# Performance work log

Measured on AMD Instinct MI355X. Metric: run time of the kernel, lower is better.

Reference implementation:

```python
import jax, jax.numpy as jnp
import numpy as np

D_STATE = 16


def setup_inputs() -> dict:
    key = jax.random.key(0)
    ks = jax.random.split(key, 7)
    B, S, D = 8, 4096, 64
    ds = D_STATE
    x = jax.random.normal(ks[0], (B, S, D), dtype=jnp.float32)
    # Selection layers modeled as Linear(d_model, out). W_A scaled small so the
    # random transition matrices are contractive over 4096 steps.
    W_A = jax.random.normal(ks[1], (D, ds * ds), dtype=jnp.float32) * 0.01
    b_A = jnp.zeros((ds * ds,), dtype=jnp.float32)
    W_B = jax.random.normal(ks[2], (D, ds * D), dtype=jnp.float32) * 0.05
    b_B = jnp.zeros((ds * D,), dtype=jnp.float32)
    W_C = jax.random.normal(ks[3], (D, ds * D), dtype=jnp.float32) * 0.05
    b_C = jnp.zeros((ds * D,), dtype=jnp.float32)
    return {"x": x, "W_A": W_A, "b_A": b_A, "W_B": W_B, "b_B": b_B,
            "W_C": W_C, "b_C": b_C}


def reference(x, W_A, b_A, W_B, b_B, W_C, b_C):
    B, S, D = x.shape
    ds = D_STATE
    # Input-dependent (selective) parameters per timestep
    A = (x @ W_A + b_A).reshape(B, S, ds, ds)      # [B,S,ds,ds]
    Bm = (x @ W_B + b_B).reshape(B, S, ds, D)      # [B,S,ds,D]
    Cm = (x @ W_C + b_C).reshape(B, S, ds, D)      # [B,S,ds,D]
    # Pre-contract B_t @ x_t once: [B,S,ds]
    Bx = jnp.einsum('bsnd,bsd->bsn', Bm, x)

    def step(h, inputs):
        A_t, Bx_t = inputs                          # [B,ds,ds], [B,ds]
        h = jnp.einsum('bij,bj->bi', A_t, h) + Bx_t
        return h, h

    h0 = jnp.zeros((B, ds), dtype=x.dtype)
    _, hs = jax.lax.scan(step, h0,
                         (jnp.swapaxes(A, 0, 1), jnp.swapaxes(Bx, 0, 1)))
    hs = jnp.swapaxes(hs, 0, 1)                     # [B,S,ds]
    # output_t = C_t^T @ h_t  -> [B,S,D]
    return jnp.einsum('bsnd,bsn->bsd', Cm, hs)
```

## Files before the change

### kernel.cpp

```cpp
#include <hip/hip_runtime.h>

#define BATCH   8
#define SEQ     4096
#define DM      64
#define DS      16
#define BS      (BATCH*SEQ)
#define CHUNK   16
#define NCHT    (BS/CHUNK)
#define SG      16
#define NSG     (NCHT/SG)

typedef __attribute__((ext_vector_type(8))) __bf16 bf16x8;
typedef __attribute__((ext_vector_type(4))) float  f32x4;

__device__ __forceinline__ unsigned short f2bf(float f) {
  unsigned int u = __float_as_uint(f);
  u += 0x7fffu + ((u >> 16) & 1u);
  return (unsigned short)(u >> 16);
}
__device__ __forceinline__ float bflo(unsigned int u) { return __uint_as_float(u << 16); }
__device__ __forceinline__ float bfhi(unsigned int u) { return __uint_as_float(u & 0xffff0000u); }

#define AS_I 20
#define AS_T 324

__global__ __launch_bounds__(256) void k0_castw(
    const float* __restrict__ WA, const float* __restrict__ WB,
    const float* __restrict__ WC,
    unsigned short* __restrict__ WAt, unsigned short* __restrict__ WBt,
    unsigned short* __restrict__ WCt)
{
  const int o = blockIdx.x * 256 + threadIdx.x;
  if (o < 16384) {
    const int c = o >> 6, e = o & 63;
    WAt[o] = f2bf(WA[e * 256 + c]);
  } else if (o < 16384 + 65536) {
    const int p = o - 16384;
    const int c = p >> 6, e = p & 63;
    WBt[p] = f2bf(WB[e * 1024 + c]);
  } else {
    const int p = o - 16384 - 65536;
    const int c = p >> 6, e = p & 63;
    WCt[p] = f2bf(WC[e * 1024 + c]);
  }
}

__global__ __launch_bounds__(128) void g1(
    const float* __restrict__ x, const unsigned short* __restrict__ WBt,
    const float* __restrict__ bB, const unsigned short* __restrict__ WAt,
    const float* __restrict__ bA, unsigned short* __restrict__ xb,
    unsigned short* __restrict__ Wt_ws, float* __restrict__ u_ws,
    float* __restrict__ P_ws, float* __restrict__ v_ws)
{
  __shared__ __align__(16) unsigned char smem[32 * AS_T * 2];
  float (*xs)[68]     = (float (*)[68])smem;
  float* bBs          = (float*)(smem + 8704);
  unsigned short* As  = (unsigned short*)smem;
  __shared__ __align__(16) float bxs[32][16];
  __shared__ __align__(16) float us[2][16];

  const int tid  = threadIdx.x;
  const int lane = tid & 63;
  const int l15  = lane & 15;
  const int quad = lane >> 4;
  const int w    = tid >> 6;
  const int t0   = blockIdx.x * 32;
  const int twl  = w * 16;

  {
    const float4* xg = (const float4*)(x + (size_t)t0 * DM);
    #pragma unroll
    for (int i = 0; i < 4; ++i) {
      const int f4 = tid + 128 * i;
      ((float4*)&xs[f4 >> 4][0])[f4 & 15] = xg[f4];
    }
    ((float4*)bBs)[tid]       = ((const float4*)bB)[tid];
    ((float4*)bBs)[tid + 128] = ((const float4*)bB)[tid + 128];
    if (tid < 32) us[tid >> 4][tid & 15] = 0.f;
  }
  __syncthreads();

  bf16x8 a0, a1;
  {
    const int row = twl + l15;
    union { bf16x8 v; ushort4 s[2]; } ua, ub;
    float4 p0 = *(const float4*)&xs[row][quad * 8];
    float4 p1 = *(const float4*)&xs[row][quad * 8 + 4];
    float4 p2 = *(const float4*)&xs[row][32 + quad * 8];
    float4 p3 = *(const float4*)&xs[row][32 + quad * 8 + 4];
    ua.s[0] = (ushort4){f2bf(p0.x), f2bf(p0.y), f2bf(p0.z), f2bf(p0.w)};
    ua.s[1] = (ushort4){f2bf(p1.x), f2bf(p1.y), f2bf(p1.z), f2bf(p1.w)};
    ub.s[0] = (ushort4){f2bf(p2.x), f2bf(p2.y), f2bf(p2.z), f2bf(p2.w)};
    ub.s[1] = (ushort4){f2bf(p3.x), f2bf(p3.y), f2bf(p3.z), f2bf(p3.w)};
    a0 = ua.v; a1 = ub.v;
    unsigned short* xp = xb + (size_t)(t0 + row) * 64 + quad * 8;
    *(bf16x8*)xp        = a0;
    *(bf16x8*)(xp + 32) = a1;
  }

  #pragma unroll 2
  for (int n = 0; n < 16; ++n) {
    f32x4 ac[4];
    #pragma unroll
    for (int r = 0; r < 4; ++r) {
      const bf16x8* wv = (const bf16x8*)(WBt + (size_t)((n * 4 + r) * 16 + l15) * 64);
      f32x4 t = {0.f, 0.f, 0.f, 0.f};
      t = __builtin_amdgcn_mfma_f32_16x16x32_bf16(a0, wv[quad],     t, 0, 0, 0);
      t = __builtin_amdgcn_mfma_f32_16x16x32_bf16(a1, wv[quad + 4], t, 0, 0, 0);
      ac[r] = t;
    }
    float part[4] = {0.f, 0.f, 0.f, 0.f};
    #pragma unroll
    for (int r = 0; r < 4; ++r) {
      const float bb = bBs[n * 64 + r * 16 + l15];
      #pragma unroll
      for (int reg = 0; reg < 4; ++reg) {
        const int tl = twl + quad * 4 + reg;
        part[reg] = fmaf(ac[r][reg] + bb, xs[tl][r * 16 + l15], part[reg]);
      }
    }
    #pragma unroll
    for (int off = 1; off < 16; off <<= 1) {
      #pragma unroll
      for (int reg = 0; reg < 4; ++reg)
        part[reg] += __shfl_xor(part[reg], off, 64);
    }
    if (l15 == 0) {
      #pragma unroll
      for (int reg = 0; reg < 4; ++reg)
        bxs[twl + quad * 4 + reg][n] = part[reg];
    }
  }
  __syncthreads();

  #pragma unroll 2
  for (int ns = 0; ns < 16; ++ns) {
    const bf16x8* wv = (const bf16x8*)(WAt + (size_t)(ns * 16 + l15) * 64);
    f32x4 acc = {0.f, 0.f, 0.f, 0.f};
    acc = __builtin_amdgcn_mfma_f32_16x16x32_bf16(a0, wv[quad],     acc, 0, 0, 0);
    acc = __builtin_amdgcn_mfma_f32_16x16x32_bf16(a1, wv[quad + 4], acc, 0, 0, 0);
    const float bias = bA[ns * 16 + l15];
    #pragma unroll
    for (int r = 0; r < 4; ++r)
      As[(twl + quad * 4 + r) * AS_T + ns * AS_I + l15] = f2bf(acc[r] + bias);
  }
  __syncthreads();

  {
    bf16x8 wb;
    #pragma unroll
    for (int j = 0; j < 8; ++j) wb[j] = (__bf16)((quad * 8 + j == l15) ? 1.f : 0.f);
    f32x4 d = {0.f, 0.f, 0.f, 0.f};
    const int qq = quad & 1;

    #pragma unroll 1
    for (int t = 0; t < CHUNK; ++t) {
      const int tl = twl + t;
      const unsigned short* rp = &As[tl * AS_T + l15 * AS_I];
      uint2 r0 = *(const uint2*)(rp);
      uint2 r1 = *(const uint2*)(rp + 4);
      uint2 r2 = *(const uint2*)(rp + 8);
      uint2 r3 = *(const uint2*)(rp + 12);

      uint4 abits;
      if (quad == 0)      abits = make_uint4(r0.x, r0.y, r1.x, r1.y);
      else if (quad == 1) abits = make_uint4(r2.x, r2.y, r3.x, r3.y);
      else                abits = make_uint4(0u, 0u, 0u, 0u);
      bf16x8 af = *(bf16x8*)&abits;

      f32x4 z4 = {0.f, 0.f, 0.f, 0.f};
      d = __builtin_amdgcn_mfma_f32_16x16x32_bf16(af, wb, z4, 0, 0, 0);

      float nu = bxs[tl][l15];
      {
        float4 U0 = *(const float4*)&us[w][0];
        float4 U1 = *(const float4*)&us[w][4];
        float4 U2 = *(const float4*)&us[w][8];
        float4 U3 = *(const float4*)&us[w][12];
        nu = fmaf(bflo(r0.x), U0.x, nu); nu = fmaf(bfhi(r0.x), U0.y, nu);
        nu = fmaf(bflo(r0.y), U0.z, nu); nu = fmaf(bfhi(r0.y), U0.w, nu);
        nu = fmaf(bflo(r1.x), U1.x, nu); nu = fmaf(bfhi(r1.x), U1.y, nu);
        nu = fmaf(bflo(r1.y), U1.z, nu); nu = fmaf(bfhi(r1.y), U1.w, nu);
        nu = fmaf(bflo(r2.x), U2.x, nu); nu = fmaf(bfhi(r2.x), U2.y, nu);
        nu = fmaf(bflo(r2.y), U2.z, nu); nu = fmaf(bfhi(r2.y), U2.w, nu);
        nu = fmaf(bflo(r3.x), U3.x, nu); nu = fmaf(bfhi(r3.x), U3.y, nu);
        nu = fmaf(bflo(r3.y), U3.z, nu); nu = fmaf(bfhi(r3.y), U3.w, nu);
      }

      bf16x8 nb;
      nb[0] = (__bf16)__shfl(d[0], (2 * qq + 0) * 16 + l15, 64);
      nb[1] = (__bf16)__shfl(d[1], (2 * qq + 0) * 16 + l15, 64);
      nb[2] = (__bf16)__shfl(d[2], (2 * qq + 0) * 16 + l15, 64);
      nb[3] = (__bf16)__shfl(d[3], (2 * qq + 0) * 16 + l15, 64);
      nb[4] = (__bf16)__shfl(d[0], (2 * qq + 1) * 16 + l15, 64);
      nb[5] = (__bf16)__shfl(d[1], (2 * qq + 1) * 16 + l15, 64);
      nb[6] = (__bf16)__shfl(d[2], (2 * qq + 1) * 16 + l15, 64);
      nb[7] = (__bf16)__shfl(d[3], (2 * qq + 1) * 16 + l15, 64);
      wb = nb;

      if (quad == 0) {
        us[w][l15] = nu;
        bxs[tl][l15] = nu;
      }
      #pragma unroll
      for (int r = 0; r < 4; ++r)
        As[tl * AS_T + (quad * 4 + r) * AS_I + l15] = f2bf(d[r]);
    }

    const int chunk = blockIdx.x * 2 + w;
    #pragma unroll
    for (int r = 0; r < 4; ++r)
      P_ws[(size_t)chunk * 256 + (quad * 4 + r) * 16 + l15] = d[r];
    if (quad == 0) v_ws[(size_t)chunk * DS + l15] = us[w][l15];
  }
  __syncthreads();

  {
    uint4* Wg = (uint4*)(Wt_ws + (size_t)t0 * 256);
    #pragma unroll 1
    for (int z = 0; z < 8; ++z) {
      const int p4 = z * 128 + tid;
      const int f  = p4 * 8;
      const int t  = f >> 8, i = (f >> 4) & 15, k = f & 15;
      const unsigned short* sp = &As[t * AS_T + i * AS_I + k];
      uint2 lo = *(const uint2*)(sp);
      uint2 hi = *(const uint2*)(sp + 4);
      Wg[p4] = make_uint4(lo.x, lo.y, hi.x, hi.y);
    }
    ((float4*)(u_ws + (size_t)t0 * DS))[tid] = ((const float4*)&bxs[0][0])[tid];
  }
}

__global__ __launch_bounds__(256) void k3a(
    const float* __restrict__ P_ws, const float* __restrict__ v_ws,
    float* __restrict__ Q_ws, float* __restrict__ w_ws)
{
  __shared__ float wsv[4][16];
  const int tid  = threadIdx.x;
  const int lane = tid & 63;
  const int l15  = lane & 15;
  const int quad = lane >> 4;
  const int wv   = tid >> 6;
  const int s    = blockIdx.x * 4 + wv;
  const int qq   = quad & 1;

  if (lane < 16) wsv[wv][lane] = 0.f;
  bf16x8 wb;
  #pragma unroll
  for (int j = 0; j < 8; ++j) wb[j] = (__bf16)((quad * 8 + j == l15) ? 1.f : 0.f);
  f32x4 d = {0.f, 0.f, 0.f, 0.f};

  #pragma unroll 1
  for (int t = 0; t < SG; ++t) {
    const int chunk = s * SG + t;
    float4 p0 = {0.f,0.f,0.f,0.f}, p1 = {0.f,0.f,0.f,0.f};
    if (quad < 2) {
      const float4* pr = (const float4*)(P_ws + (size_t)chunk * 256 + l15 * 16 + quad * 8);
      p0 = pr[0]; p1 = pr[1];
    }
    bf16x8 af;
    af[0] = (__bf16)p0.x; af[1] = (__bf16)p0.y; af[2] = (__bf16)p0.z; af[3] = (__bf16)p0.w;
    af[4] = (__bf16)p1.x; af[5] = (__bf16)p1.y; af[6] = (__bf16)p1.z; af[7] = (__bf16)p1.w;

    f32x4 z4 = {0.f, 0.f, 0.f, 0.f};
    d = __builtin_amdgcn_mfma_f32_16x16x32_bf16(af, wb, z4, 0, 0, 0);

    float part = 0.f;
    if (quad < 2) {
      const float* wrow = &wsv[wv][quad * 8];
      part = p0.x*wrow[0] + p0.y*wrow[1] + p0.z*wrow[2] + p0.w*wrow[3]
           + p1.x*wrow[4] + p1.y*wrow[5] + p1.z*wrow[6] + p1.w*wrow[7];
    }
    part += __shfl_xor(part, 16, 64);
    const float nv = v_ws[(size_t)chunk * DS + l15];

    bf16x8 nb;
    nb[0] = (__bf16)__shfl(d[0], (2 * qq + 0) * 16 + l15, 64);
    nb[1] = (__bf16)__shfl(d[1], (2 * qq + 0) * 16 + l15, 64);
    nb[2] = (__bf16)__shfl(d[2], (2 * qq + 0) * 16 + l15, 64);
    nb[3] = (__bf16)__shfl(d[3], (2 * qq + 0) * 16 + l15, 64);
    nb[4] = (__bf16)__shfl(d[0], (2 * qq + 1) * 16 + l15, 64);
    nb[5] = (__bf16)__shfl(d[1], (2 * qq + 1) * 16 + l15, 64);
    nb[6] = (__bf16)__shfl(d[2], (2 * qq + 1) * 16 + l15, 64);
    nb[7] = (__bf16)__shfl(d[3], (2 * qq + 1) * 16 + l15, 64);
    wb = nb;

    if (quad == 0) wsv[wv][l15] = part + nv;
  }

  #pragma unroll
  for (int r = 0; r < 4; ++r)
    Q_ws[(size_t)s * 256 + (quad * 4 + r) * 16 + l15] = d[r];
  if (quad == 0) w_ws[(size_t)s * DS + l15] = wsv[wv][l15];
}

__global__ __launch_bounds__(128) void k3b(
    const float* __restrict__ Q_ws, const float* __restrict__ w_ws,
    float* __restrict__ hbg_ws)
{
  const int tid = threadIdx.x;
  const int b = tid >> 4;
  const int r = tid & 15;
  float h = 0.f;

  #pragma unroll 1
  for (int g = 0; g < 16; ++g) {
    const int s = b * 16 + g;
    const float4* Pr = (const float4*)&Q_ws[(size_t)s * 256 + r * 16];
    float4 c0 = Pr[0], c1 = Pr[1], c2 = Pr[2], c3 = Pr[3];
    const float vc = w_ws[(size_t)s * DS + r];
    hbg_ws[(size_t)s * DS + r] = h;
    float acc = vc;
    acc += c0.x*__shfl(h, 0,16) + c0.y*__shfl(h, 1,16) + c0.z*__shfl(h, 2,16) + c0.w*__shfl(h, 3,16);
    acc += c1.x*__shfl(h, 4,16) + c1.y*__shfl(h, 5,16) + c1.z*__shfl(h, 6,16) + c1.w*__shfl(h, 7,16);
    acc += c2.x*__shfl(h, 8,16) + c2.y*__shfl(h, 9,16) + c2.z*__shfl(h,10,16) + c2.w*__shfl(h,11,16);
    acc += c3.x*__shfl(h,12,16) + c3.y*__shfl(h,13,16) + c3.z*__shfl(h,14,16) + c3.w*__shfl(h,15,16);
    h = acc;
  }
}

__global__ __launch_bounds__(256) void k3c(
    const float* __restrict__ P_ws, const float* __restrict__ v_ws,
    const float* __restrict__ hbg_ws, float* __restrict__ hb_ws)
{
  const int tid = threadIdx.x;
  const int s = blockIdx.x * 16 + (tid >> 4);
  const int r = tid & 15;
  float h = hbg_ws[(size_t)s * DS + r];

  #pragma unroll 1
  for (int t = 0; t < SG; ++t) {
    const int chunk = s * SG + t;
    const float4* Pr = (const float4*)&P_ws[(size_t)chunk * 256 + r * 16];
    float4 c0 = Pr[0], c1 = Pr[1], c2 = Pr[2], c3 = Pr[3];
    const float vc = v_ws[(size_t)chunk * DS + r];
    hb_ws[(size_t)chunk * DS + r] = h;
    float acc = vc;
    acc += c0.x*__shfl(h, 0,16) + c0.y*__shfl(h, 1,16) + c0.z*__shfl(h, 2,16) + c0.w*__shfl(h, 3,16);
    acc += c1.x*__shfl(h, 4,16) + c1.y*__shfl(h, 5,16) + c1.z*__shfl(h, 6,16) + c1.w*__shfl(h, 7,16);
    acc += c2.x*__shfl(h, 8,16) + c2.y*__shfl(h, 9,16) + c2.z*__shfl(h,10,16) + c2.w*__shfl(h,11,16);
    acc += c3.x*__shfl(h,12,16) + c3.y*__shfl(h,13,16) + c3.z*__shfl(h,14,16) + c3.w*__shfl(h,15,16);
    h = acc;
  }
}

__global__ __launch_bounds__(256) void g2(
    const unsigned short* __restrict__ xb, const unsigned short* __restrict__ WCt,
    const float* __restrict__ bC, const unsigned short* __restrict__ Wt_ws,
    const float* __restrict__ u_ws, const float* __restrict__ hb_ws,
    float* __restrict__ out)
{
  __shared__ float hsh[64][17];
  __shared__ float bCs[1024];
  const int tid  = threadIdx.x;
  const int lane = tid & 63;
  const int l15  = lane & 15;
  const int quad = lane >> 4;
  const int w    = tid >> 6;
  const int t0   = blockIdx.x * 64;
  const int twl  = w * 16;

  ((float4*)bCs)[tid] = ((const float4*)bC)[tid];

  #pragma unroll
  for (int z = 0; z < 4; ++z) {
    const int gcell = z * 256 + tid;
    const int tl = gcell >> 4, i = gcell & 15;
    const int t = t0 + tl;
    const uint4* wr = (const uint4*)(Wt_ws + (size_t)t * 256 + i * 16);
    uint4 wa = wr[0], wbv = wr[1];
    const float4* hp = (const float4*)(hb_ws + (size_t)(t >> 4) * DS);
    float4 h0 = hp[0], h1 = hp[1], h2 = hp[2], h3 = hp[3];
    float acc = u_ws[(size_t)t * DS + i];
    acc = fmaf(bflo(wa.x),  h0.x, acc); acc = fmaf(bfhi(wa.x),  h0.y, acc);
    acc = fmaf(bflo(wa.y),  h0.z, acc); acc = fmaf(bfhi(wa.y),  h0.w, acc);
    acc = fmaf(bflo(wa.z),  h1.x, acc); acc = fmaf(bfhi(wa.z),  h1.y, acc);
    acc = fmaf(bflo(wa.w),  h1.z, acc); acc = fmaf(bfhi(wa.w),  h1.w, acc);
    acc = fmaf(bflo(wbv.x), h2.x, acc); acc = fmaf(bfhi(wbv.x), h2.y, acc);
    acc = fmaf(bflo(wbv.y), h2.z, acc); acc = fmaf(bfhi(wbv.y), h2.w, acc);
    acc = fmaf(bflo(wbv.z), h3.x, acc); acc = fmaf(bfhi(wbv.z), h3.y, acc);
    acc = fmaf(bflo(wbv.w), h3.z, acc); acc = fmaf(bfhi(wbv.w), h3.w, acc);
    hsh[tl][i] = acc;
  }

  const bf16x8* xv = (const bf16x8*)(xb + (size_t)(t0 + twl + l15) * 64);
  bf16x8 a0 = xv[quad];
  bf16x8 a1 = xv[quad + 4];
  __syncthreads();

  f32x4 ota[4];
  #pragma unroll
  for (int r = 0; r < 4; ++r) ota[r] = (f32x4){0.f, 0.f, 0.f, 0.f};

  #pragma unroll 2
  for (int n = 0; n < 16; ++n) {
    f32x4 ac[4];
    #pragma unroll
    for (int r = 0; r < 4; ++r) {
      const bf16x8* wv = (const bf16x8*)(WCt + (size_t)((n * 4 + r) * 16 + l15) * 64);
      f32x4 t = {0.f, 0.f, 0.f, 0.f};
      t = __builtin_amdgcn_mfma_f32_16x16x32_bf16(a0, wv[quad],     t, 0, 0, 0);
      t = __builtin_amdgcn_mfma_f32_16x16x32_bf16(a1, wv[quad + 4], t, 0, 0, 0);
      ac[r] = t;
    }
    float hn[4];
    #pragma unroll
    for (int reg = 0; reg < 4; ++reg) hn[reg] = hsh[twl + quad * 4 + reg][n];
    #pragma unroll
    for (int r = 0; r < 4; ++r) {
      const float bc = bCs[n * 64 + r * 16 + l15];
      #pragma unroll
      for (int reg = 0; reg < 4; ++reg)
        ota[r][reg] = fmaf(ac[r][reg] + bc, hn[reg], ota[r][reg]);
    }
  }

  #pragma unroll
  for (int r = 0; r < 4; ++r)
    #pragma unroll
    for (int reg = 0; reg < 4; ++reg)
      out[(size_t)(t0 + twl + quad * 4 + reg) * DM + r * 16 + l15] = ota[r][reg];
}

extern "C" void kernel_launch(void* const* d_in, const int* in_sizes, int n_in,
                              void* d_out, int out_size, void* d_ws, size_t ws_size,
                              hipStream_t stream) {
  const float* x  = (const float*)d_in[0];
  const float* WA = (const float*)d_in[1];
  const float* bA = (const float*)d_in[2];
  const float* WB = (const float*)d_in[3];
  const float* bB = (const float*)d_in[4];
  const float* WC = (const float*)d_in[5];
  const float* bC = (const float*)d_in[6];
  float* out = (float*)d_out;

  float* ws     = (float*)d_ws;
  float* P_ws   = ws;
  float* v_ws   = P_ws   + (size_t)NCHT * 256;
  float* u_ws   = v_ws   + (size_t)NCHT * DS;
  float* Q_ws   = u_ws   + (size_t)BS * DS;
  float* w_ws   = Q_ws   + (size_t)NSG * 256;
  float* hbg_ws = w_ws   + (size_t)NSG * DS;
  float* hb_ws  = hbg_ws + (size_t)NSG * DS;
  unsigned short* xb    = (unsigned short*)(hb_ws + (size_t)NCHT * DS);
  unsigned short* WAt   = xb  + (size_t)BS * 64;
  unsigned short* WBt   = WAt + 256 * 64;
  unsigned short* WCt   = WBt + 1024 * 64;
  unsigned short* Wt_ws = WCt + 1024 * 64;

  k0_castw<<<576,      256, 0, stream>>>(WA, WB, WC, WAt, WBt, WCt);
  g1      <<<BS / 32,  128, 0, stream>>>(x, WBt, bB, WAt, bA, xb, Wt_ws, u_ws, P_ws, v_ws);
  k3a     <<<NSG / 4,  256, 0, stream>>>(P_ws, v_ws, Q_ws, w_ws);
  k3b     <<<1,        128, 0, stream>>>(Q_ws, w_ws, hbg_ws);
  k3c     <<<NSG / 16, 256, 0, stream>>>(P_ws, v_ws, hbg_ws, hb_ws);
  g2      <<<BS / 64,  256, 0, stream>>>(xb, WCt, bC, Wt_ws, u_ws, hb_ws, out);
}
```

Baseline: 182.7 us.

## Software-pipeline weight and state loads across all kernels, fuse A and B projection loops

Adds register double-buffering of weight fragments in g1 and g2, so the next iteration's global loads are issued before the current MFMAs, and merges the A-projection loop into the B loop in g1, which removes a barrier. The scan kernels (g1 inner loop, k3a, k3b, k3c) prefetch the next step's operands and split serial FMA chains into independent partial sums to shorten the dependency chain. Launch bounds change occupancy hints, and g1's shared memory is no longer aliased, which raises LDS use. The risks are higher register pressure and changed floating-point summation order.

```diff
diff --git a/kernel.cpp b/kernel.cpp
--- a/kernel.cpp
+++ b/kernel.cpp
@@ -45,17 +45,41 @@
   }
 }
 
-__global__ __launch_bounds__(128) void g1(
+struct WFrag {
+  bf16x8 b00, b01, b10, b11, b20, b21, b30, b31;
+  bf16x8 a0f, a1f;
+  float  ba;
+};
+
+__device__ __forceinline__ WFrag loadw(
+    const unsigned short* __restrict__ WBt, const unsigned short* __restrict__ WAt,
+    const float* __restrict__ bA, int n, int l15, int quad)
+{
+  WFrag f;
+  const bf16x8* w0 = (const bf16x8*)(WBt + (size_t)((n * 4 + 0) * 16 + l15) * 64);
+  const bf16x8* w1 = (const bf16x8*)(WBt + (size_t)((n * 4 + 1) * 16 + l15) * 64);
+  const bf16x8* w2 = (const bf16x8*)(WBt + (size_t)((n * 4 + 2) * 16 + l15) * 64);
+  const bf16x8* w3 = (const bf16x8*)(WBt + (size_t)((n * 4 + 3) * 16 + l15) * 64);
+  f.b00 = w0[quad]; f.b01 = w0[quad + 4];
+  f.b10 = w1[quad]; f.b11 = w1[quad + 4];
+  f.b20 = w2[quad]; f.b21 = w2[quad + 4];
+  f.b30 = w3[quad]; f.b31 = w3[quad + 4];
+  const bf16x8* wa = (const bf16x8*)(WAt + (size_t)(n * 16 + l15) * 64);
+  f.a0f = wa[quad]; f.a1f = wa[quad + 4];
+  f.ba  = bA[n * 16 + l15];
+  return f;
+}
+
+__global__ __launch_bounds__(128, 2) void g1(
     const float* __restrict__ x, const unsigned short* __restrict__ WBt,
     const float* __restrict__ bB, const unsigned short* __restrict__ WAt,
     const float* __restrict__ bA, unsigned short* __restrict__ xb,
     unsigned short* __restrict__ Wt_ws, float* __restrict__ u_ws,
     float* __restrict__ P_ws, float* __restrict__ v_ws)
 {
-  __shared__ __align__(16) unsigned char smem[32 * AS_T * 2];
-  float (*xs)[68]     = (float (*)[68])smem;
-  float* bBs          = (float*)(smem + 8704);
-  unsigned short* As  = (unsigned short*)smem;
+  __shared__ __align__(16) float xs[32][68];
+  __shared__ __align__(16) float bBs[1024];
+  __shared__ __align__(16) unsigned short As[32 * AS_T];
   __shared__ __align__(16) float bxs[32][16];
   __shared__ __align__(16) float us[2][16];
 
@@ -79,6 +103,8 @@
     if (tid < 32) us[tid >> 4][tid & 15] = 0.f;
   }
   __syncthreads();
+
+  WFrag cur = loadw(WBt, WAt, bA, 0, l15, quad);
 
   bf16x8 a0, a1;
   {
@@ -98,26 +124,44 @@
     *(bf16x8*)(xp + 32) = a1;
   }
 
-  #pragma unroll 2
+  float xv[4][4];
+  #pragma unroll
+  for (int r = 0; r < 4; ++r)
+    #pragma unroll
+    for (int reg = 0; reg < 4; ++reg)
+      xv[r][reg] = xs[twl + quad * 4 + reg][r * 16 + l15];
+
+  #pragma unroll
   for (int n = 0; n < 16; ++n) {
-    f32x4 ac[4];
-    #pragma unroll
-    for (int r = 0; r < 4; ++r) {
-      const bf16x8* wv = (const bf16x8*)(WBt + (size_t)((n * 4 + r) * 16 + l15) * 64);
-      f32x4 t = {0.f, 0.f, 0.f, 0.f};
-      t = __builtin_amdgcn_mfma_f32_16x16x32_bf16(a0, wv[quad],     t, 0, 0, 0);
-      t = __builtin_amdgcn_mfma_f32_16x16x32_bf16(a1, wv[quad + 4], t, 0, 0, 0);
-      ac[r] = t;
-    }
-    float part[4] = {0.f, 0.f, 0.f, 0.f};
-    #pragma unroll
-    for (int r = 0; r < 4; ++r) {
-      const float bb = bBs[n * 64 + r * 16 + l15];
-      #pragma unroll
-      for (int reg = 0; reg < 4; ++reg) {
-        const int tl = twl + quad * 4 + reg;
-        part[reg] = fmaf(ac[r][reg] + bb, xs[tl][r * 16 + l15], part[reg]);
-      }
+    WFrag nxt = (n < 15) ? loadw(WBt, WAt, bA, n + 1, l15, quad) : cur;
+
+    const f32x4 z4 = {0.f, 0.f, 0.f, 0.f};
+    f32x4 aac = z4;
+    aac = __builtin_amdgcn_mfma_f32_16x16x32_bf16(a0, cur.a0f, aac, 0, 0, 0);
+    aac = __builtin_amdgcn_mfma_f32_16x16x32_bf16(a1, cur.a1f, aac, 0, 0, 0);
+
+    f32x4 ac0 = z4, ac1 = z4, ac2 = z4, ac3 = z4;
+    ac0 = __builtin_amdgcn_mfma_f32_16x16x32_bf16(a0, cur.b00, ac0, 0, 0, 0);
+    ac0 = __builtin_amdgcn_mfma_f32_16x16x32_bf16(a1, cur.b01, ac0, 0, 0, 0);
+    ac1 = __builtin_amdgcn_mfma_f32_16x16x32_bf16(a0, cur.b10, ac1, 0, 0, 0);
+    ac1 = __builtin_amdgcn_mfma_f32_16x16x32_bf16(a1, cur.b11, ac1, 0, 0, 0);
+    ac2 = __builtin_amdgcn_mfma_f32_16x16x32_bf16(a0, cur.b20, ac2, 0, 0, 0);
+    ac2 = __builtin_amdgcn_mfma_f32_16x16x32_bf16(a1, cur.b21, ac2, 0, 0, 0);
+    ac3 = __builtin_amdgcn_mfma_f32_16x16x32_bf16(a0, cur.b30, ac3, 0, 0, 0);
+    ac3 = __builtin_amdgcn_mfma_f32_16x16x32_bf16(a1, cur.b31, ac3, 0, 0, 0);
+
+    const float bb0 = bBs[n * 64 +  0 + l15];
+    const float bb1 = bBs[n * 64 + 16 + l15];
+    const float bb2 = bBs[n * 64 + 32 + l15];
+    const float bb3 = bBs[n * 64 + 48 + l15];
+    float part[4];
+    #pragma unroll
+    for (int reg = 0; reg < 4; ++reg) {
+      float s = fmaf(ac0[reg] + bb0, xv[0][reg], 0.f);
+      s = fmaf(ac1[reg] + bb1, xv[1][reg], s);
+      s = fmaf(ac2[reg] + bb2, xv[2][reg], s);
+      s = fmaf(ac3[reg] + bb3, xv[3][reg], s);
+      part[reg] = s;
     }
     #pragma unroll
     for (int off = 1; off < 16; off <<= 1) {
@@ -130,21 +174,14 @@
       for (int reg = 0; reg < 4; ++reg)
         bxs[twl + quad * 4 + reg][n] = part[reg];
     }
-  }
-  __syncthreads();
-
-  #pragma unroll 2
-  for (int ns = 0; ns < 16; ++ns) {
-    const bf16x8* wv = (const bf16x8*)(WAt + (size_t)(ns * 16 + l15) * 64);
-    f32x4 acc = {0.f, 0.f, 0.f, 0.f};
-    acc = __builtin_amdgcn_mfma_f32_16x16x32_bf16(a0, wv[quad],     acc, 0, 0, 0);
-    acc = __builtin_amdgcn_mfma_f32_16x16x32_bf16(a1, wv[quad + 4], acc, 0, 0, 0);
-    const float bias = bA[ns * 16 + l15];
-    #pragma unroll
-    for (int r = 0; r < 4; ++r)
-      As[(twl + quad * 4 + r) * AS_T + ns * AS_I + l15] = f2bf(acc[r] + bias);
-  }
-  __syncthreads();
+
+    As[(twl + quad * 4 + 0) * AS_T + n * AS_I + l15] = f2bf(aac[0] + cur.ba);
+    As[(twl + quad * 4 + 1) * AS_T + n * AS_I + l15] = f2bf(aac[1] + cur.ba);
+    As[(twl + quad * 4 + 2) * AS_T + n * AS_I + l15] = f2bf(aac[2] + cur.ba);
+    As[(twl + quad * 4 + 3) * AS_T + n * AS_I + l15] = f2bf(aac[3] + cur.ba);
+
+    cur = nxt;
+  }
 
   {
     bf16x8 wb;
@@ -153,14 +190,24 @@
     f32x4 d = {0.f, 0.f, 0.f, 0.f};
     const int qq = quad & 1;
 
+    const unsigned short* rpp = &As[twl * AS_T + l15 * AS_I];
+    uint2 r0 = *(const uint2*)(rpp);
+    uint2 r1 = *(const uint2*)(rpp + 4);
+    uint2 r2 = *(const uint2*)(rpp + 8);
+    uint2 r3 = *(const uint2*)(rpp + 12);
+
     #pragma unroll 1
     for (int t = 0; t < CHUNK; ++t) {
       const int tl = twl + t;
-      const unsigned short* rp = &As[tl * AS_T + l15 * AS_I];
-      uint2 r0 = *(const uint2*)(rp);
-      uint2 r1 = *(const uint2*)(rp + 4);
-      uint2 r2 = *(const uint2*)(rp + 8);
-      uint2 r3 = *(const uint2*)(rp + 12);
+
+      uint2 s0, s1, s2, s3;
+      if (t < CHUNK - 1) {
+        const unsigned short* rp = &As[(tl + 1) * AS_T + l15 * AS_I];
+        s0 = *(const uint2*)(rp);
+        s1 = *(const uint2*)(rp + 4);
+        s2 = *(const uint2*)(rp + 8);
+        s3 = *(const uint2*)(rp + 12);
+      } else { s0 = r0; s1 = r1; s2 = r2; s3 = r3; }
 
       uint4 abits;
       if (quad == 0)      abits = make_uint4(r0.x, r0.y, r1.x, r1.y);
@@ -171,20 +218,22 @@
       f32x4 z4 = {0.f, 0.f, 0.f, 0.f};
       d = __builtin_amdgcn_mfma_f32_16x16x32_bf16(af, wb, z4, 0, 0, 0);
 
-      float nu = bxs[tl][l15];
+      float nu;
       {
         float4 U0 = *(const float4*)&us[w][0];
         float4 U1 = *(const float4*)&us[w][4];
         float4 U2 = *(const float4*)&us[w][8];
         float4 U3 = *(const float4*)&us[w][12];
-        nu = fmaf(bflo(r0.x), U0.x, nu); nu = fmaf(bfhi(r0.x), U0.y, nu);
-        nu = fmaf(bflo(r0.y), U0.z, nu); nu = fmaf(bfhi(r0.y), U0.w, nu);
-        nu = fmaf(bflo(r1.x), U1.x, nu); nu = fmaf(bfhi(r1.x), U1.y, nu);
-        nu = fmaf(bflo(r1.y), U1.z, nu); nu = fmaf(bfhi(r1.y), U1.w, nu);
-        nu = fmaf(bflo(r2.x), U2.x, nu); nu = fmaf(bfhi(r2.x), U2.y, nu);
-        nu = fmaf(bflo(r2.y), U2.z, nu); nu = fmaf(bfhi(r2.y), U2.w, nu);
-        nu = fmaf(bflo(r3.x), U3.x, nu); nu = fmaf(bfhi(r3.x), U3.y, nu);
-        nu = fmaf(bflo(r3.y), U3.z, nu); nu = fmaf(bfhi(r3.y), U3.w, nu);
+        float n0 = bxs[tl][l15], n1 = 0.f, n2 = 0.f, n3 = 0.f;
+        n0 = fmaf(bflo(r0.x), U0.x, n0); n0 = fmaf(bfhi(r0.x), U0.y, n0);
+        n0 = fmaf(bflo(r0.y), U0.z, n0); n0 = fmaf(bfhi(r0.y), U0.w, n0);
+        n1 = fmaf(bflo(r1.x), U1.x, n1); n1 = fmaf(bfhi(r1.x), U1.y, n1);
+        n1 = fmaf(bflo(r1.y), U1.z, n1); n1 = fmaf(bfhi(r1.y), U1.w, n1);
+        n2 = fmaf(bflo(r2.x), U2.x, n2); n2 = fmaf(bfhi(r2.x), U2.y, n2);
+        n2 = fmaf(bflo(r2.y), U2.z, n2); n2 = fmaf(bfhi(r2.y), U2.w, n2);
+        n3 = fmaf(bflo(r3.x), U3.x, n3); n3 = fmaf(bfhi(r3.x), U3.y, n3);
+        n3 = fmaf(bflo(r3.y), U3.z, n3); n3 = fmaf(bfhi(r3.y), U3.w, n3);
+        nu = (n0 + n1) + (n2 + n3);
       }
 
       bf16x8 nb;
@@ -205,6 +254,8 @@
       #pragma unroll
       for (int r = 0; r < 4; ++r)
         As[tl * AS_T + (quad * 4 + r) * AS_I + l15] = f2bf(d[r]);
+
+      r0 = s0; r1 = s1; r2 = s2; r3 = s3;
     }
 
     const int chunk = blockIdx.x * 2 + w;
@@ -231,7 +282,7 @@
   }
 }
 
-__global__ __launch_bounds__(256) void k3a(
+__global__ __launch_bounds__(256, 1) void k3a(
     const float* __restrict__ P_ws, const float* __restrict__ v_ws,
     float* __restrict__ Q_ws, float* __restrict__ w_ws)
 {
@@ -250,14 +301,30 @@
   for (int j = 0; j < 8; ++j) wb[j] = (__bf16)((quad * 8 + j == l15) ? 1.f : 0.f);
   f32x4 d = {0.f, 0.f, 0.f, 0.f};
 
-  #pragma unroll 1
-  for (int t = 0; t < SG; ++t) {
-    const int chunk = s * SG + t;
-    float4 p0 = {0.f,0.f,0.f,0.f}, p1 = {0.f,0.f,0.f,0.f};
+  float4 p0 = {0.f,0.f,0.f,0.f}, p1 = {0.f,0.f,0.f,0.f};
+  float nv;
+  {
+    const int chunk = s * SG;
     if (quad < 2) {
       const float4* pr = (const float4*)(P_ws + (size_t)chunk * 256 + l15 * 16 + quad * 8);
       p0 = pr[0]; p1 = pr[1];
     }
+    nv = v_ws[(size_t)chunk * DS + l15];
+  }
+
+  #pragma unroll 1
+  for (int t = 0; t < SG; ++t) {
+    float4 q0 = {0.f,0.f,0.f,0.f}, q1 = {0.f,0.f,0.f,0.f};
+    float nv2 = 0.f;
+    if (t < SG - 1) {
+      const int chunk = s * SG + t + 1;
+      if (quad < 2) {
+        const float4* pr = (const float4*)(P_ws + (size_t)chunk * 256 + l15 * 16 + quad * 8);
+        q0 = pr[0]; q1 = pr[1];
+      }
+      nv2 = v_ws[(size_t)chunk * DS + l15];
+    }
+
     bf16x8 af;
     af[0] = (__bf16)p0.x; af[1] = (__bf16)p0.y; af[2] = (__bf16)p0.z; af[3] = (__bf16)p0.w;
     af[4] = (__bf16)p1.x; af[5] = (__bf16)p1.y; af[6] = (__bf16)p1.z; af[7] = (__bf16)p1.w;
@@ -272,7 +339,6 @@
            + p1.x*wrow[4] + p1.y*wrow[5] + p1.z*wrow[6] + p1.w*wrow[7];
     }
     part += __shfl_xor(part, 16, 64);
-    const float nv = v_ws[(size_t)chunk * DS + l15];
 
     bf16x8 nb;
     nb[0] = (__bf16)__shfl(d[0], (2 * qq + 0) * 16 + l15, 64);
@@ -286,6 +352,8 @@
     wb = nb;
 
     if (quad == 0) wsv[wv][l15] = part + nv;
+
+    p0 = q0; p1 = q1; nv = nv2;
   }
 
   #pragma unroll
@@ -294,7 +362,7 @@
   if (quad == 0) w_ws[(size_t)s * DS + l15] = wsv[wv][l15];
 }
 
-__global__ __launch_bounds__(128) void k3b(
+__global__ __launch_bounds__(128, 1) void k3b(
     const float* __restrict__ Q_ws, const float* __restrict__ w_ws,
     float* __restrict__ hbg_ws)
 {
@@ -303,23 +371,36 @@
   const int r = tid & 15;
   float h = 0.f;
 
+  float4 c0, c1, c2, c3; float vc;
+  {
+    const int s = b * 16;
+    const float4* Pr = (const float4*)&Q_ws[(size_t)s * 256 + r * 16];
+    c0 = Pr[0]; c1 = Pr[1]; c2 = Pr[2]; c3 = Pr[3];
+    vc = w_ws[(size_t)s * DS + r];
+  }
+
   #pragma unroll 1
   for (int g = 0; g < 16; ++g) {
     const int s = b * 16 + g;
-    const float4* Pr = (const float4*)&Q_ws[(size_t)s * 256 + r * 16];
-    float4 c0 = Pr[0], c1 = Pr[1], c2 = Pr[2], c3 = Pr[3];
-    const float vc = w_ws[(size_t)s * DS + r];
+    float4 d0, d1, d2, d3; float vc2;
+    if (g < 15) {
+      const float4* Pr = (const float4*)&Q_ws[(size_t)(s + 1) * 256 + r * 16];
+      d0 = Pr[0]; d1 = Pr[1]; d2 = Pr[2]; d3 = Pr[3];
+      vc2 = w_ws[(size_t)(s + 1) * DS + r];
+    } else { d0 = c0; d1 = c1; d2 = c2; d3 = c3; vc2 = vc; }
+
     hbg_ws[(size_t)s * DS + r] = h;
-    float acc = vc;
-    acc += c0.x*__shfl(h, 0,16) + c0.y*__shfl(h, 1,16) + c0.z*__shfl(h, 2,16) + c0.w*__shfl(h, 3,16);
-    acc += c1.x*__shfl(h, 4,16) + c1.y*__shfl(h, 5,16) + c1.z*__shfl(h, 6,16) + c1.w*__shfl(h, 7,16);
-    acc += c2.x*__shfl(h, 8,16) + c2.y*__shfl(h, 9,16) + c2.z*__shfl(h,10,16) + c2.w*__shfl(h,11,16);
-    acc += c3.x*__shfl(h,12,16) + c3.y*__shfl(h,13,16) + c3.z*__shfl(h,14,16) + c3.w*__shfl(h,15,16);
-    h = acc;
-  }
-}
-
-__global__ __launch_bounds__(256) void k3c(
+    float a0 = c0.x*__shfl(h, 0,16) + c0.y*__shfl(h, 1,16) + c0.z*__shfl(h, 2,16) + c0.w*__shfl(h, 3,16);
+    float a1 = c1.x*__shfl(h, 4,16) + c1.y*__shfl(h, 5,16) + c1.z*__shfl(h, 6,16) + c1.w*__shfl(h, 7,16);
+    float a2 = c2.x*__shfl(h, 8,16) + c2.y*__shfl(h, 9,16) + c2.z*__shfl(h,10,16) + c2.w*__shfl(h,11,16);
+    float a3 = c3.x*__shfl(h,12,16) + c3.y*__shfl(h,13,16) + c3.z*__shfl(h,14,16) + c3.w*__shfl(h,15,16);
+    h = vc + ((a0 + a1) + (a2 + a3));
+
+    c0 = d0; c1 = d1; c2 = d2; c3 = d3; vc = vc2;
+  }
+}
+
+__global__ __launch_bounds__(256, 1) void k3c(
     const float* __restrict__ P_ws, const float* __restrict__ v_ws,
     const float* __restrict__ hbg_ws, float* __restrict__ hb_ws)
 {
@@ -328,23 +409,55 @@
   const int r = tid & 15;
   float h = hbg_ws[(size_t)s * DS + r];
 
+  float4 c0, c1, c2, c3; float vc;
+  {
+    const int chunk = s * SG;
+    const float4* Pr = (const float4*)&P_ws[(size_t)chunk * 256 + r * 16];
+    c0 = Pr[0]; c1 = Pr[1]; c2 = Pr[2]; c3 = Pr[3];
+    vc = v_ws[(size_t)chunk * DS + r];
+  }
+
   #pragma unroll 1
   for (int t = 0; t < SG; ++t) {
     const int chunk = s * SG + t;
-    const float4* Pr = (const float4*)&P_ws[(size_t)chunk * 256 + r * 16];
-    float4 c0 = Pr[0], c1 = Pr[1], c2 = Pr[2], c3 = Pr[3];
-    const float vc = v_ws[(size_t)chunk * DS + r];
+    float4 d0, d1, d2, d3; float vc2;
+    if (t < SG - 1) {
+      const float4* Pr = (const float4*)&P_ws[(size_t)(chunk + 1) * 256 + r * 16];
+      d0 = Pr[0]; d1 = Pr[1]; d2 = Pr[2]; d3 = Pr[3];
+      vc2 = v_ws[(size_t)(chunk + 1) * DS + r];
+    } else { d0 = c0; d1 = c1; d2 = c2; d3 = c3; vc2 = vc; }
+
     hb_ws[(size_t)chunk * DS + r] = h;
-    float acc = vc;
-    acc += c0.x*__shfl(h, 0,16) + c0.y*__shfl(h, 1,16) + c0.z*__shfl(h, 2,16) + c0.w*__shfl(h, 3,16);
-    acc += c1.x*__shfl(h, 4,16) + c1.y*__shfl(h, 5,16) + c1.z*__shfl(h, 6,16) + c1.w*__shfl(h, 7,16);
-    acc += c2.x*__shfl(h, 8,16) + c2.y*__shfl(h, 9,16) + c2.z*__shfl(h,10,16) + c2.w*__shfl(h,11,16);
-    acc += c3.x*__shfl(h,12,16) + c3.y*__shfl(h,13,16) + c3.z*__shfl(h,14,16) + c3.w*__shfl(h,15,16);
-    h = acc;
-  }
-}
-
-__global__ __launch_bounds__(256) void g2(
+    float a0 = c0.x*__shfl(h, 0,16) + c0.y*__shfl(h, 1,16) + c0.z*__shfl(h, 2,16) + c0.w*__shfl(h, 3,16);
+    float a1 = c1.x*__shfl(h, 4,16) + c1.y*__shfl(h, 5,16) + c1.z*__shfl(h, 6,16) + c1.w*__shfl(h, 7,16);
+    float a2 = c2.x*__shfl(h, 8,16) + c2.y*__shfl(h, 9,16) + c2.z*__shfl(h,10,16) + c2.w*__shfl(h,11,16);
+    float a3 = c3.x*__shfl(h,12,16) + c3.y*__shfl(h,13,16) + c3.z*__shfl(h,14,16) + c3.w*__shfl(h,15,16);
+    h = vc + ((a0 + a1) + (a2 + a3));
+
+    c0 = d0; c1 = d1; c2 = d2; c3 = d3; vc = vc2;
+  }
+}
+
+struct CFrag {
+  bf16x8 c00, c01, c10, c11, c20, c21, c30, c31;
+};
+
+__device__ __forceinline__ CFrag loadc(
+    const unsigned short* __restrict__ WCt, int n, int l15, int quad)
+{
+  CFrag f;
+  const bf16x8* w0 = (const bf16x8*)(WCt + (size_t)((n * 4 + 0) * 16 + l15) * 64);
+  const bf16x8* w1 = (const bf16x8*)(WCt + (size_t)((n * 4 + 1) * 16 + l15) * 64);
+  const bf16x8* w2 = (const bf16x8*)(WCt + (size_t)((n * 4 + 2) * 16 + l15) * 64);
+  const bf16x8* w3 = (const bf16x8*)(WCt + (size_t)((n * 4 + 3) * 16 + l15) * 64);
+  f.c00 = w0[quad]; f.c01 = w0[quad + 4];
+  f.c10 = w1[quad]; f.c11 = w1[quad + 4];
+  f.c20 = w2[quad]; f.c21 = w2[quad + 4];
+  f.c30 = w3[quad]; f.c31 = w3[quad + 4];
+  return f;
+}
+
+__global__ __launch_bounds__(256, 2) void g2(
     const unsigned short* __restrict__ xb, const unsigned short* __restrict__ WCt,
     const float* __restrict__ bC, const unsigned short* __restrict__ Wt_ws,
     const float* __restrict__ u_ws, const float* __restrict__ hb_ws,
@@ -362,57 +475,78 @@
 
   ((float4*)bCs)[tid] = ((const float4*)bC)[tid];
 
+  const bf16x8* xvp = (const bf16x8*)(xb + (size_t)(t0 + twl + l15) * 64);
+  bf16x8 a0 = xvp[quad];
+  bf16x8 a1 = xvp[quad + 4];
+
+  uint4 wA[4], wB[4]; float uac[4]; float4 hh[4][4];
   #pragma unroll
   for (int z = 0; z < 4; ++z) {
     const int gcell = z * 256 + tid;
     const int tl = gcell >> 4, i = gcell & 15;
     const int t = t0 + tl;
     const uint4* wr = (const uint4*)(Wt_ws + (size_t)t * 256 + i * 16);
-    uint4 wa = wr[0], wbv = wr[1];
+    wA[z] = wr[0]; wB[z] = wr[1];
     const float4* hp = (const float4*)(hb_ws + (size_t)(t >> 4) * DS);
-    float4 h0 = hp[0], h1 = hp[1], h2 = hp[2], h3 = hp[3];
-    float acc = u_ws[(size_t)t * DS + i];
-    acc = fmaf(bflo(wa.x),  h0.x, acc); acc = fmaf(bfhi(wa.x),  h0.y, acc);
-    acc = fmaf(bflo(wa.y),  h0.z, acc); acc = fmaf(bfhi(wa.y),  h0.w, acc);
-    acc = fmaf(bflo(wa.z),  h1.x, acc); acc = fmaf(bfhi(wa.z),  h1.y, acc);
-    acc = fmaf(bflo(wa.w),  h1.z, acc); acc = fmaf(bfhi(wa.w),  h1.w, acc);
-    acc = fmaf(bflo(wbv.x), h2.x, acc); acc = fmaf(bfhi(wbv.x), h2.y, acc);
-    acc = fmaf(bflo(wbv.y), h2.z, acc); acc = fmaf(bfhi(wbv.y), h2.w, acc);
-    acc = fmaf(bflo(wbv.z), h3.x, acc); acc = fmaf(bfhi(wbv.z), h3.y, acc);
-    acc = fmaf(bflo(wbv.w), h3.z, acc); acc = fmaf(bfhi(wbv.w), h3.w, acc);
-    hsh[tl][i] = acc;
-  }
-
-  const bf16x8* xv = (const bf16x8*)(xb + (size_t)(t0 + twl + l15) * 64);
-  bf16x8 a0 = xv[quad];
-  bf16x8 a1 = xv[quad + 4];
+    hh[z][0] = hp[0]; hh[z][1] = hp[1]; hh[z][2] = hp[2]; hh[z][3] = hp[3];
+    uac[z] = u_ws[(size_t)t * DS + i];
+  }
+  #pragma unroll
+  for (int z = 0; z < 4; ++z) {
+    const int gcell = z * 256 + tid;
+    const int tl = gcell >> 4, i = gcell & 15;
+    uint4 wa = wA[z], wbv = wB[z];
+    float4 h0 = hh[z][0], h1 = hh[z][1], h2 = hh[z][2], h3 = hh[z][3];
+    float p0 = uac[z], p1 = 0.f, p2 = 0.f, p3 = 0.f;
+    p0 = fmaf(bflo(wa.x),  h0.x, p0); p0 = fmaf(bfhi(wa.x),  h0.y, p0);
+    p0 = fmaf(bflo(wa.y),  h0.z, p0); p0 = fmaf(bfhi(wa.y),  h0.w, p0);
+    p1 = fmaf(bflo(wa.z),  h1.x, p1); p1 = fmaf(bfhi(wa.z),  h1.y, p1);
+    p1 = fmaf(bflo(wa.w),  h1.z, p1); p1 = fmaf(bfhi(wa.w),  h1.w, p1);
+    p2 = fmaf(bflo(wbv.x), h2.x, p2); p2 = fmaf(bfhi(wbv.x), h2.y, p2);
+    p2 = fmaf(bflo(wbv.y), h2.z, p2); p2 = fmaf(bfhi(wbv.y), h2.w, p2);
+    p3 = fmaf(bflo(wbv.z), h3.x, p3); p3 = fmaf(bfhi(wbv.z), h3.y, p3);
+    p3 = fmaf(bflo(wbv.w), h3.z, p3); p3 = fmaf(bfhi(wbv.w), h3.w, p3);
+    hsh[tl][i] = (p0 + p1) + (p2 + p3);
+  }
   __syncthreads();
 
   f32x4 ota[4];
   #pragma unroll
   for (int r = 0; r < 4; ++r) ota[r] = (f32x4){0.f, 0.f, 0.f, 0.f};
 
-  #pragma unroll 2
+  CFrag cur = loadc(WCt, 0, l15, quad);
+  #pragma unroll
   for (int n = 0; n < 16; ++n) {
-    f32x4 ac[4];
-    #pragma unroll
-    for (int r = 0; r < 4; ++r) {
-      const bf16x8* wv = (const bf16x8*)(WCt + (size_t)((n * 4 + r) * 16 + l15) * 64);
-      f32x4 t = {0.f, 0.f, 0.f, 0.f};
-      t = __builtin_amdgcn_mfma_f32_16x16x32_bf16(a0, wv[quad],     t, 0, 0, 0);
-      t = __builtin_amdgcn_mfma_f32_16x16x32_bf16(a1, wv[quad + 4], t, 0, 0, 0);
-      ac[r] = t;
-    }
+    CFrag nxt = (n < 15) ? loadc(WCt, n + 1, l15, quad) : cur;
+
+    const f32x4 z4 = {0.f, 0.f, 0.f, 0.f};
+    f32x4 ac0 = z4, ac1 = z4, ac2 = z4, ac3 = z4;
+    ac0 = __builtin_amdgcn_mfma_f32_16x16x32_bf16(a0, cur.c00, ac0, 0, 0, 0);
+    ac0 = __builtin_amdgcn_mfma_f32_16x16x32_bf16(a1, cur.c01, ac0, 0, 0, 0);
+    ac1 = __builtin_amdgcn_mfma_f32_16x16x32_bf16(a0, cur.c10, ac1, 0, 0, 0);
+    ac1 = __builtin_amdgcn_mfma_f32_16x16x32_bf16(a1, cur.c11, ac1, 0, 0, 0);
+    ac2 = __builtin_amdgcn_mfma_f32_16x16x32_bf16(a0, cur.c20, ac2, 0, 0, 0);
+    ac2 = __builtin_amdgcn_mfma_f32_16x16x32_bf16(a1, cur.c21, ac2, 0, 0, 0);
+    ac3 = __builtin_amdgcn_mfma_f32_16x16x32_bf16(a0, cur.c30, ac3, 0, 0, 0);
+    ac3 = __builtin_amdgcn_mfma_f32_16x16x32_bf16(a1, cur.c31, ac3, 0, 0, 0);
+
     float hn[4];
     #pragma unroll
     for (int reg = 0; reg < 4; ++reg) hn[reg] = hsh[twl + quad * 4 + reg][n];
-    #pragma unroll
-    for (int r = 0; r < 4; ++r) {
-      const float bc = bCs[n * 64 + r * 16 + l15];
-      #pragma unroll
-      for (int reg = 0; reg < 4; ++reg)
-        ota[r][reg] = fmaf(ac[r][reg] + bc, hn[reg], ota[r][reg]);
-    }
+
+    const float bc0 = bCs[n * 64 +  0 + l15];
+    const float bc1 = bCs[n * 64 + 16 + l15];
+    const float bc2 = bCs[n * 64 + 32 + l15];
+    const float bc3 = bCs[n * 64 + 48 + l15];
+    #pragma unroll
+    for (int reg = 0; reg < 4; ++reg) {
+      ota[0][reg] = fmaf(ac0[reg] + bc0, hn[reg], ota[0][reg]);
+      ota[1][reg] = fmaf(ac1[reg] + bc1, hn[reg], ota[1][reg]);
+      ota[2][reg] = fmaf(ac2[reg] + bc2, hn[reg], ota[2][reg]);
+      ota[3][reg] = fmaf(ac3[reg] + bc3, hn[reg], ota[3][reg]);
+    }
+
+    cur = nxt;
   }
 
   #pragma unroll
```

New measurement: 197.0 us. +7.8%, slower.
